# Performance work log

Measured on AMD Instinct MI355X. Metric: run time of the kernel, lower is better.

Reference implementation:

```python
import jax, jax.numpy as jnp
import numpy as np

B, OUT, IN = 4096, 1024, 1024
BN_EPS = 1e-5


def setup_inputs() -> dict:
    key = jax.random.key(0)
    kx, k1, k2, k3 = jax.random.split(key, 4)
    # kaiming_uniform_ with a=sqrt(5): bound = sqrt(6 / ((1+a^2) * fan_in)) = 1/sqrt(fan_in)
    bound = 1.0 / np.sqrt(IN)
    x = jax.random.normal(kx, (B, IN), dtype=jnp.float32)
    c1 = jax.random.uniform(k1, (OUT, IN), jnp.float32, -bound, bound)
    c2 = jax.random.uniform(k2, (OUT, IN), jnp.float32, -bound, bound)
    c3 = jax.random.uniform(k3, (OUT, IN), jnp.float32, -bound, bound)
    bias = jnp.zeros((OUT, IN), jnp.float32)
    gamma = jnp.ones((OUT,), jnp.float32)   # BatchNorm1d weight
    beta = jnp.zeros((OUT,), jnp.float32)   # BatchNorm1d bias
    return {"x": x, "c1": c1, "c2": c2, "c3": c3, "bias": bias,
            "gamma": gamma, "beta": beta}


def reference(x, c1, c2, c3, bias, gamma, beta):
    # Fused polynomial 'matmul': out[b,o] = sum_i x*c1 + x^2*c2 + x^3*c3 + bias
    x2 = x * x
    x3 = x2 * x
    y = (jnp.einsum('bi,oi->bo', x, c1)
         + jnp.einsum('bi,oi->bo', x2, c2)
         + jnp.einsum('bi,oi->bo', x3, c3)
         + jnp.sum(bias, axis=1))  # bias reduced over in_features
    # BatchNorm1d (training mode: batch statistics, biased variance)
    mean = jnp.mean(y, axis=0)
    var = jnp.var(y, axis=0)
    return (y - mean) * jax.lax.rsqrt(var + BN_EPS) * gamma + beta
```

## Files before the change

kernel.cpp:

```cpp
#include <hip/hip_runtime.h>
#include <stdint.h>

#define B_ROWS 4096
#define OUTF   1024
#define INF    1024
#define KTOT   3072
#define BN_EPS 1e-5f
#define BM 128
#define BN 128
#define BK 64
#define NSTEP (KTOT / BK)

typedef short  short8  __attribute__((ext_vector_type(8)));
typedef float  floatx4 __attribute__((ext_vector_type(4)));

struct alignas(8) s4 { short x, y, z, w; };

#define WAIT_VM4 0x0F74
#define WAIT_VM2 0x0F72
#define WAIT_VM0 0x0F70

__device__ __forceinline__ short f2bf(float f) {
  union { float f; uint32_t u; } cv; cv.f = f;
  uint32_t u = cv.u;
  uint32_t r = (u + 0x7fffu + ((u >> 16) & 1u)) >> 16;
  return (short)r;
}

__device__ __forceinline__ void load_lds16(const void* g, void* l) {
  __builtin_amdgcn_global_load_lds(
      (const __attribute__((address_space(1))) uint32_t*)(uintptr_t)g,
      (__attribute__((address_space(3))) uint32_t*)(uint32_t)(uintptr_t)l,
      16, 0, 0);
}

__global__ void prep_all(const float4* __restrict__ x4,
                         const float4* __restrict__ c1, const float4* __restrict__ c2,
                         const float4* __restrict__ c3,
                         short* __restrict__ Xb, short* __restrict__ Wb) {
  int b = blockIdx.x;
  if (b < 4096) {
    int idx = b * 256 + threadIdx.x;
    float4 v = x4[idx];
    int row = idx >> 8;
    int c   = (idx & 255) << 2;
    size_t base = (size_t)row * KTOT + c;
    s4 p1 = { f2bf(v.x), f2bf(v.y), f2bf(v.z), f2bf(v.w) };
    float ax = v.x * v.x, ay = v.y * v.y, az = v.z * v.z, aw = v.w * v.w;
    s4 p2 = { f2bf(ax), f2bf(ay), f2bf(az), f2bf(aw) };
    s4 p3 = { f2bf(ax * v.x), f2bf(ay * v.y), f2bf(az * v.z), f2bf(aw * v.w) };
    *(s4*)&Xb[base]        = p1;
    *(s4*)&Xb[base + 1024] = p2;
    *(s4*)&Xb[base + 2048] = p3;
  } else {
    int idx = (b - 4096) * 256 + threadIdx.x;
    int row = idx >> 8;
    int c   = (idx & 255) << 2;
    size_t base = (size_t)row * KTOT + c;
    float4 a = c1[idx], bb = c2[idx], d = c3[idx];
    s4 p1 = { f2bf(a.x),  f2bf(a.y),  f2bf(a.z),  f2bf(a.w)  };
    s4 p2 = { f2bf(bb.x), f2bf(bb.y), f2bf(bb.z), f2bf(bb.w) };
    s4 p3 = { f2bf(d.x),  f2bf(d.y),  f2bf(d.z),  f2bf(d.w)  };
    *(s4*)&Wb[base]        = p1;
    *(s4*)&Wb[base + 1024] = p2;
    *(s4*)&Wb[base + 2048] = p3;
  }
}

__global__ __launch_bounds__(1024, 4) void gemm_poly(
    const short* __restrict__ Xb, const short* __restrict__ Wb,
    float* __restrict__ Y, float* __restrict__ psum, float* __restrict__ psq) {
  __shared__ __align__(16) short As[4][BM * BK];
  __shared__ __align__(16) short Bs[4][BN * BK];
  const int tid  = threadIdx.x;
  const int lane = tid & 63;
  const int wave = tid >> 6;
  const int wr = wave >> 2;
  const int wc = wave & 3;
  const int lb  = blockIdx.x;
  const int xcd = lb & 7;
  const int sl  = lb >> 3;
  const int bx  = sl & 7;
  const int by  = xcd * 4 + (sl >> 3);
  const int row0 = by * BM;
  const int col0 = bx * BN;
  const short* Ag = Xb + (size_t)row0 * KTOT;
  const short* Bg = Wb + (size_t)col0 * KTOT;
  const int frag_m = lane & 15;
  const int sel = lane >> 4;
  floatx4 acc[2][2] = {};

  const int soff = (tid >> 3) * KTOT + ((tid & 7) ^ ((tid >> 3) & 7)) * 8;
  const int ldst = tid * 8;

  #pragma unroll
  for (int t = 0; t < 3; ++t) {
    load_lds16(Ag + soff + t * BK, &As[t][ldst]);
    load_lds16(Bg + soff + t * BK, &Bs[t][ldst]);
  }

#define GSTEP(CUR, PRE, KT_PRE, DO_PRE, WAITIMM)                              \
  {                                                                           \
    __builtin_amdgcn_s_waitcnt(WAITIMM);                                      \
    __builtin_amdgcn_s_barrier();                                             \
    if (DO_PRE) {                                                             \
      load_lds16(Ag + soff + (KT_PRE), &As[PRE][ldst]);                       \
      load_lds16(Bg + soff + (KT_PRE), &Bs[PRE][ldst]);                       \
    }                                                                         \
    _Pragma("unroll")                                                         \
    for (int s = 0; s < 2; ++s) {                                             \
      short8 af[2], bfr[2];                                                   \
      _Pragma("unroll")                                                       \
      for (int i = 0; i < 2; ++i) {                                           \
        int r = wr * 32 + i * 16 + frag_m;                                    \
        int p = (s * 4 + sel) ^ (r & 7);                                      \
        af[i] = *(const short8*)&As[CUR][r * BK + p * 8];                     \
      }                                                                       \
      _Pragma("unroll")                                                       \
      for (int j = 0; j < 2; ++j) {                                           \
        int r = wc * 32 + j * 16 + frag_m;                                    \
        int p = (s * 4 + sel) ^ (r & 7);                                      \
        bfr[j] = *(const short8*)&Bs[CUR][r * BK + p * 8];                    \
      }                                                                       \
      _Pragma("unroll")                                                       \
      for (int i = 0; i < 2; ++i)                                             \
        _Pragma("unroll")                                                     \
        for (int j = 0; j < 2; ++j)                                           \
          acc[i][j] = __builtin_amdgcn_mfma_f32_16x16x32_bf16(                \
              af[i], bfr[j], acc[i][j], 0, 0, 0);                             \
    }                                                                         \
  }

  for (int t4 = 0; t4 < 44; t4 += 4) {
    GSTEP(0, 3, (t4 + 3) * BK, 1, WAIT_VM4);
    GSTEP(1, 0, (t4 + 4) * BK, 1, WAIT_VM4);
    GSTEP(2, 1, (t4 + 5) * BK, 1, WAIT_VM4);
    GSTEP(3, 2, (t4 + 6) * BK, 1, WAIT_VM4);
  }
  GSTEP(0, 3, 47 * BK, 1, WAIT_VM4);
  GSTEP(1, 0, 0, 0, WAIT_VM4);
  GSTEP(2, 0, 0, 0, WAIT_VM2);
  GSTEP(3, 0, 0, 0, WAIT_VM0);
#undef GSTEP

  float* colred = (float*)&As[0][0];
  float sv[2] = {0.f, 0.f}, sq[2] = {0.f, 0.f};
  #pragma unroll
  for (int j = 0; j < 2; ++j)
    #pragma unroll
    for (int i = 0; i < 2; ++i)
      #pragma unroll
      for (int r = 0; r < 4; ++r) {
        float v = acc[i][j][r];
        sv[j] += v; sq[j] += v * v;
      }
  #pragma unroll
  for (int j = 0; j < 2; ++j) {
    sv[j] += __shfl_xor(sv[j], 16, 64); sv[j] += __shfl_xor(sv[j], 32, 64);
    sq[j] += __shfl_xor(sq[j], 16, 64); sq[j] += __shfl_xor(sq[j], 32, 64);
  }
  if (sel == 0) {
    #pragma unroll
    for (int j = 0; j < 2; ++j) {
      int cc = wc * 32 + j * 16 + frag_m;
      colred[(wr * 2 + 0) * 128 + cc] = sv[j];
      colred[(wr * 2 + 1) * 128 + cc] = sq[j];
    }
  }
  #pragma unroll
  for (int j = 0; j < 2; ++j) {
    int gc = col0 + wc * 32 + j * 16 + frag_m;
    #pragma unroll
    for (int i = 0; i < 2; ++i) {
      int gr = row0 + wr * 32 + i * 16 + sel * 4;
      #pragma unroll
      for (int r = 0; r < 4; ++r)
        Y[(size_t)(gr + r) * OUTF + gc] = acc[i][j][r];
    }
  }
  __syncthreads();
  if (tid < BN) {
    float s0 = colred[0 * 128 + tid] + colred[2 * 128 + tid]
             + colred[4 * 128 + tid] + colred[6 * 128 + tid];
    float s1 = colred[1 * 128 + tid] + colred[3 * 128 + tid]
             + colred[5 * 128 + tid] + colred[7 * 128 + tid];
    psum[(size_t)by * OUTF + col0 + tid] = s0;
    psq [(size_t)by * OUTF + col0 + tid] = s1;
  }
}

__global__ void bn_fused(const float* __restrict__ psum, const float* __restrict__ psq,
                         const float* __restrict__ gamma, const float* __restrict__ beta,
                         float* __restrict__ Y) {
  __shared__ float sc[32], sh[32];
  const int c0 = blockIdx.x * 32;
  const int t = threadIdx.x;
  if (t < 32) {
    float s = 0.f, s2 = 0.f;
    #pragma unroll 8
    for (int p = 0; p < 32; ++p) {
      s  += psum[p * OUTF + c0 + t];
      s2 += psq [p * OUTF + c0 + t];
    }
    float mean = s * (1.0f / B_ROWS);
    float var  = s2 * (1.0f / B_ROWS) - mean * mean;
    float scale = gamma[c0 + t] * rsqrtf(var + BN_EPS);
    sc[t] = scale;
    sh[t] = beta[c0 + t] - mean * scale;
  }
  __syncthreads();
  const int f4c = t & 7;
  const int rr  = t >> 3;
  const int row0 = blockIdx.y * 256;
  float4* Y4 = (float4*)Y;
  const int cb = f4c * 4;
  float s0 = sc[cb], s1 = sc[cb+1], s2 = sc[cb+2], s3 = sc[cb+3];
  float h0 = sh[cb], h1 = sh[cb+1], h2 = sh[cb+2], h3 = sh[cb+3];
  #pragma unroll
  for (int it = 0; it < 8; ++it) {
    int row = row0 + it * 32 + rr;
    size_t idx = (size_t)row * 256 + (c0 >> 2) + f4c;
    float4 v = Y4[idx];
    v.x = v.x * s0 + h0; v.y = v.y * s1 + h1;
    v.z = v.z * s2 + h2; v.w = v.w * s3 + h3;
    Y4[idx] = v;
  }
}

extern "C" void kernel_launch(void* const* d_in, const int* in_sizes, int n_in,
                              void* d_out, int out_size, void* d_ws, size_t ws_size,
                              hipStream_t stream) {
  const float* x     = (const float*)d_in[0];
  const float* c1    = (const float*)d_in[1];
  const float* c2    = (const float*)d_in[2];
  const float* c3    = (const float*)d_in[3];
  const float* gamma = (const float*)d_in[5];
  const float* beta  = (const float*)d_in[6];
  float* out = (float*)d_out;
  char* ws = (char*)d_ws;

  short* Xb   = (short*)(ws);
  short* Wb   = (short*)(ws + 25165824);
  float* psum = (float*)(ws + 31457280);
  float* psq  = (float*)(ws + 31588352);

  prep_all<<<5120, 256, 0, stream>>>((const float4*)x, (const float4*)c1,
                                     (const float4*)c2, (const float4*)c3,
                                     Xb, Wb);

  gemm_poly<<<256, 1024, 0, stream>>>(Xb, Wb, out, psum, psq);

  dim3 bgrid(OUTF / 32, B_ROWS / 256);
  bn_fused<<<bgrid, 256, 0, stream>>>(psum, psq, gamma, beta, out);
}
```

Before: 123.7 us.

## Halve GEMM block threads with larger per-wave tiles and bf16 intermediate Y

The GEMM block drops from 16 waves to 8, each computing a 64x32 tile with 8 accumulators, so every wave reuses more fragments per LDS read and issues twice as many async global-to-LDS loads per stage (wait counts adjusted). The pre-normalisation Y is now written as bf16 to a workspace buffer and read back by the BN kernel, which halves the intermediate traffic. In exchange there are fewer waves per CU to hide latency, and the output picks up a bf16 rounding error before normalisation.

```diff
diff --git a/kernel.cpp b/kernel.cpp
--- a/kernel.cpp
+++ b/kernel.cpp
@@ -9,15 +9,14 @@
 #define BM 128
 #define BN 128
 #define BK 64
-#define NSTEP (KTOT / BK)
 
 typedef short  short8  __attribute__((ext_vector_type(8)));
 typedef float  floatx4 __attribute__((ext_vector_type(4)));
 
 struct alignas(8) s4 { short x, y, z, w; };
 
+#define WAIT_VM8 0x0F78
 #define WAIT_VM4 0x0F74
-#define WAIT_VM2 0x0F72
 #define WAIT_VM0 0x0F70
 
 __device__ __forceinline__ short f2bf(float f) {
@@ -25,6 +24,11 @@
   uint32_t u = cv.u;
   uint32_t r = (u + 0x7fffu + ((u >> 16) & 1u)) >> 16;
   return (short)r;
+}
+
+__device__ __forceinline__ float bf2f(unsigned short s) {
+  union { uint32_t u; float f; } cv; cv.u = ((uint32_t)s) << 16;
+  return cv.f;
 }
 
 __device__ __forceinline__ void load_lds16(const void* g, void* l) {
@@ -67,9 +71,10 @@
   }
 }
 
-__global__ __launch_bounds__(1024, 4) void gemm_poly(
+__global__ __launch_bounds__(512, 2) void gemm_poly(
     const short* __restrict__ Xb, const short* __restrict__ Wb,
-    float* __restrict__ Y, float* __restrict__ psum, float* __restrict__ psq) {
+    unsigned short* __restrict__ Yb, float* __restrict__ psum,
+    float* __restrict__ psq) {
   __shared__ __align__(16) short As[4][BM * BK];
   __shared__ __align__(16) short Bs[4][BN * BK];
   const int tid  = threadIdx.x;
@@ -88,15 +93,22 @@
   const short* Bg = Wb + (size_t)col0 * KTOT;
   const int frag_m = lane & 15;
   const int sel = lane >> 4;
-  floatx4 acc[2][2] = {};
-
-  const int soff = (tid >> 3) * KTOT + ((tid & 7) ^ ((tid >> 3) & 7)) * 8;
-  const int ldst = tid * 8;
+  floatx4 acc[4][2] = {};
+
+  int soff[2], ldst[2];
+  #pragma unroll
+  for (int q = 0; q < 2; ++q) {
+    int c = tid + q * 512;
+    soff[q] = (c >> 3) * KTOT + ((c & 7) ^ ((c >> 3) & 7)) * 8;
+    ldst[q] = c * 8;
+  }
 
   #pragma unroll
   for (int t = 0; t < 3; ++t) {
-    load_lds16(Ag + soff + t * BK, &As[t][ldst]);
-    load_lds16(Bg + soff + t * BK, &Bs[t][ldst]);
+    load_lds16(Ag + soff[0] + t * BK, &As[t][ldst[0]]);
+    load_lds16(Ag + soff[1] + t * BK, &As[t][ldst[1]]);
+    load_lds16(Bg + soff[0] + t * BK, &Bs[t][ldst[0]]);
+    load_lds16(Bg + soff[1] + t * BK, &Bs[t][ldst[1]]);
   }
 
 #define GSTEP(CUR, PRE, KT_PRE, DO_PRE, WAITIMM)                              \
@@ -104,15 +116,17 @@
     __builtin_amdgcn_s_waitcnt(WAITIMM);                                      \
     __builtin_amdgcn_s_barrier();                                             \
     if (DO_PRE) {                                                             \
-      load_lds16(Ag + soff + (KT_PRE), &As[PRE][ldst]);                       \
-      load_lds16(Bg + soff + (KT_PRE), &Bs[PRE][ldst]);                       \
+      load_lds16(Ag + soff[0] + (KT_PRE), &As[PRE][ldst[0]]);                 \
+      load_lds16(Ag + soff[1] + (KT_PRE), &As[PRE][ldst[1]]);                 \
+      load_lds16(Bg + soff[0] + (KT_PRE), &Bs[PRE][ldst[0]]);                 \
+      load_lds16(Bg + soff[1] + (KT_PRE), &Bs[PRE][ldst[1]]);                 \
     }                                                                         \
     _Pragma("unroll")                                                         \
     for (int s = 0; s < 2; ++s) {                                             \
-      short8 af[2], bfr[2];                                                   \
+      short8 af[4], bfr[2];                                                   \
       _Pragma("unroll")                                                       \
-      for (int i = 0; i < 2; ++i) {                                           \
-        int r = wr * 32 + i * 16 + frag_m;                                    \
+      for (int i = 0; i < 4; ++i) {                                           \
+        int r = wr * 64 + i * 16 + frag_m;                                    \
         int p = (s * 4 + sel) ^ (r & 7);                                      \
         af[i] = *(const short8*)&As[CUR][r * BK + p * 8];                     \
       }                                                                       \
@@ -123,7 +137,7 @@
         bfr[j] = *(const short8*)&Bs[CUR][r * BK + p * 8];                    \
       }                                                                       \
       _Pragma("unroll")                                                       \
-      for (int i = 0; i < 2; ++i)                                             \
+      for (int i = 0; i < 4; ++i)                                             \
         _Pragma("unroll")                                                     \
         for (int j = 0; j < 2; ++j)                                           \
           acc[i][j] = __builtin_amdgcn_mfma_f32_16x16x32_bf16(                \
@@ -132,14 +146,14 @@
   }
 
   for (int t4 = 0; t4 < 44; t4 += 4) {
-    GSTEP(0, 3, (t4 + 3) * BK, 1, WAIT_VM4);
-    GSTEP(1, 0, (t4 + 4) * BK, 1, WAIT_VM4);
-    GSTEP(2, 1, (t4 + 5) * BK, 1, WAIT_VM4);
-    GSTEP(3, 2, (t4 + 6) * BK, 1, WAIT_VM4);
-  }
-  GSTEP(0, 3, 47 * BK, 1, WAIT_VM4);
-  GSTEP(1, 0, 0, 0, WAIT_VM4);
-  GSTEP(2, 0, 0, 0, WAIT_VM2);
+    GSTEP(0, 3, (t4 + 3) * BK, 1, WAIT_VM8);
+    GSTEP(1, 0, (t4 + 4) * BK, 1, WAIT_VM8);
+    GSTEP(2, 1, (t4 + 5) * BK, 1, WAIT_VM8);
+    GSTEP(3, 2, (t4 + 6) * BK, 1, WAIT_VM8);
+  }
+  GSTEP(0, 3, 47 * BK, 1, WAIT_VM8);
+  GSTEP(1, 0, 0, 0, WAIT_VM8);
+  GSTEP(2, 0, 0, 0, WAIT_VM4);
   GSTEP(3, 0, 0, 0, WAIT_VM0);
 #undef GSTEP
 
@@ -148,7 +162,7 @@
   #pragma unroll
   for (int j = 0; j < 2; ++j)
     #pragma unroll
-    for (int i = 0; i < 2; ++i)
+    for (int i = 0; i < 4; ++i)
       #pragma unroll
       for (int r = 0; r < 4; ++r) {
         float v = acc[i][j][r];
@@ -171,19 +185,17 @@
   for (int j = 0; j < 2; ++j) {
     int gc = col0 + wc * 32 + j * 16 + frag_m;
     #pragma unroll
-    for (int i = 0; i < 2; ++i) {
-      int gr = row0 + wr * 32 + i * 16 + sel * 4;
+    for (int i = 0; i < 4; ++i) {
+      int gr = row0 + wr * 64 + i * 16 + sel * 4;
       #pragma unroll
       for (int r = 0; r < 4; ++r)
-        Y[(size_t)(gr + r) * OUTF + gc] = acc[i][j][r];
+        Yb[(size_t)(gr + r) * OUTF + gc] = (unsigned short)f2bf(acc[i][j][r]);
     }
   }
   __syncthreads();
   if (tid < BN) {
-    float s0 = colred[0 * 128 + tid] + colred[2 * 128 + tid]
-             + colred[4 * 128 + tid] + colred[6 * 128 + tid];
-    float s1 = colred[1 * 128 + tid] + colred[3 * 128 + tid]
-             + colred[5 * 128 + tid] + colred[7 * 128 + tid];
+    float s0 = colred[0 * 128 + tid] + colred[2 * 128 + tid];
+    float s1 = colred[1 * 128 + tid] + colred[3 * 128 + tid];
     psum[(size_t)by * OUTF + col0 + tid] = s0;
     psq [(size_t)by * OUTF + col0 + tid] = s1;
   }
@@ -191,7 +203,8 @@
 
 __global__ void bn_fused(const float* __restrict__ psum, const float* __restrict__ psq,
                          const float* __restrict__ gamma, const float* __restrict__ beta,
-                         float* __restrict__ Y) {
+                         const unsigned short* __restrict__ Yb,
+                         float* __restrict__ out) {
   __shared__ float sc[32], sh[32];
   const int c0 = blockIdx.x * 32;
   const int t = threadIdx.x;
@@ -209,21 +222,29 @@
     sh[t] = beta[c0 + t] - mean * scale;
   }
   __syncthreads();
-  const int f4c = t & 7;
-  const int rr  = t >> 3;
+  const int sl8 = t & 3;
+  const int rr  = t >> 2;
   const int row0 = blockIdx.y * 256;
-  float4* Y4 = (float4*)Y;
-  const int cb = f4c * 4;
-  float s0 = sc[cb], s1 = sc[cb+1], s2 = sc[cb+2], s3 = sc[cb+3];
-  float h0 = sh[cb], h1 = sh[cb+1], h2 = sh[cb+2], h3 = sh[cb+3];
-  #pragma unroll
-  for (int it = 0; it < 8; ++it) {
-    int row = row0 + it * 32 + rr;
-    size_t idx = (size_t)row * 256 + (c0 >> 2) + f4c;
-    float4 v = Y4[idx];
-    v.x = v.x * s0 + h0; v.y = v.y * s1 + h1;
-    v.z = v.z * s2 + h2; v.w = v.w * s3 + h3;
-    Y4[idx] = v;
+  float s_[8], h_[8];
+  #pragma unroll
+  for (int e = 0; e < 8; ++e) { s_[e] = sc[sl8 * 8 + e]; h_[e] = sh[sl8 * 8 + e]; }
+  float4* O4 = (float4*)out;
+  #pragma unroll
+  for (int it = 0; it < 4; ++it) {
+    int row = row0 + it * 64 + rr;
+    short8 v = *(const short8*)&Yb[(size_t)row * OUTF + c0 + sl8 * 8];
+    float4 o0, o1;
+    o0.x = bf2f((unsigned short)v[0]) * s_[0] + h_[0];
+    o0.y = bf2f((unsigned short)v[1]) * s_[1] + h_[1];
+    o0.z = bf2f((unsigned short)v[2]) * s_[2] + h_[2];
+    o0.w = bf2f((unsigned short)v[3]) * s_[3] + h_[3];
+    o1.x = bf2f((unsigned short)v[4]) * s_[4] + h_[4];
+    o1.y = bf2f((unsigned short)v[5]) * s_[5] + h_[5];
+    o1.z = bf2f((unsigned short)v[6]) * s_[6] + h_[6];
+    o1.w = bf2f((unsigned short)v[7]) * s_[7] + h_[7];
+    size_t fi = (size_t)row * 256 + (c0 >> 2) + sl8 * 2;
+    O4[fi]     = o0;
+    O4[fi + 1] = o1;
   }
 }
 
@@ -239,17 +260,18 @@
   float* out = (float*)d_out;
   char* ws = (char*)d_ws;
 
-  short* Xb   = (short*)(ws);
-  short* Wb   = (short*)(ws + 25165824);
-  float* psum = (float*)(ws + 31457280);
-  float* psq  = (float*)(ws + 31588352);
+  short* Xb            = (short*)(ws);
+  short* Wb            = (short*)(ws + 25165824);
+  unsigned short* Yb   = (unsigned short*)(ws + 31457280);
+  float* psum          = (float*)(ws + 39845888);
+  float* psq           = (float*)(ws + 39976960);
 
   prep_all<<<5120, 256, 0, stream>>>((const float4*)x, (const float4*)c1,
                                      (const float4*)c2, (const float4*)c3,
                                      Xb, Wb);
 
-  gemm_poly<<<256, 1024, 0, stream>>>(Xb, Wb, out, psum, psq);
+  gemm_poly<<<256, 512, 0, stream>>>(Xb, Wb, Yb, psum, psq);
 
   dim3 bgrid(OUTF / 32, B_ROWS / 256);
-  bn_fused<<<bgrid, 256, 0, stream>>>(psum, psq, gamma, beta, out);
-}
+  bn_fused<<<bgrid, 256, 0, stream>>>(psum, psq, gamma, beta, Yb, out);
+}
```

After: 125.5 us. About the same (+1.5%).
